# Kernel tuning notes

Measured on AMD Instinct MI355X. Metric: run time of the kernel, lower is better.

The kernel has to match this reference:

```python
import jax, jax.numpy as jnp
import numpy as np

N_NODES = 50000
N_EDGES = 640000
D_IN = 128
D_H1 = 128
D_H2 = 128
N_CLASSES = 64


def setup_inputs() -> dict:
    key = jax.random.key(0)
    ks = jax.random.split(key, 8)
    x = jax.random.normal(ks[0], (N_NODES, D_IN), dtype=jnp.float32)
    edge_index = jax.random.randint(ks[1], (2, N_EDGES), 0, N_NODES, dtype=jnp.int64)
    s1 = 1.0 / np.sqrt(D_IN)
    s2 = 1.0 / np.sqrt(D_H1)
    s3 = 1.0 / np.sqrt(D_H2)
    W1 = jax.random.uniform(ks[2], (D_IN, D_H1), jnp.float32, -s1, s1)
    b1 = jnp.zeros((D_H1,), jnp.float32)
    W2 = jax.random.uniform(ks[3], (D_H1, D_H2), jnp.float32, -s2, s2)
    b2 = jnp.zeros((D_H2,), jnp.float32)
    Wl = jax.random.uniform(ks[4], (D_H2, N_CLASSES), jnp.float32, -s3, s3)
    bl = jax.random.uniform(ks[5], (N_CLASSES,), jnp.float32, -s3, s3)
    return {"x": x, "edge_index": edge_index, "W1": W1, "b1": b1,
            "W2": W2, "b2": b2, "Wl": Wl, "bl": bl}


def _gcn_norm(edge_index, num_nodes):
    # PyG GCNConv: add self-loops, symmetric normalization D^-1/2 (A+I) D^-1/2
    loop = jnp.arange(num_nodes, dtype=edge_index.dtype)
    src = jnp.concatenate([edge_index[0], loop])
    dst = jnp.concatenate([edge_index[1], loop])
    deg = jax.ops.segment_sum(jnp.ones_like(dst, dtype=jnp.float32), dst,
                              num_segments=num_nodes)
    dinv = jnp.where(deg > 0, jax.lax.rsqrt(deg), 0.0)
    norm = dinv[src] * dinv[dst]  # [E+N]
    return src, dst, norm


def _gcn_conv(h, src, dst, norm, W, b, num_nodes):
    h = h @ W                       # transform first (smaller gather when D_out small)
    msg = h[src] * norm[:, None]    # gather + per-edge scale  [E+N, D_out]
    agg = jax.ops.segment_sum(msg, dst, num_segments=num_nodes)  # scatter-add
    return agg + b


def reference(x, edge_index, W1, b1, W2, b2, Wl, bl):
    n = x.shape[0]
    src, dst, norm = _gcn_norm(edge_index, n)
    h = jax.nn.relu(_gcn_conv(x, src, dst, norm, W1, b1, n))
    # dropout is identity in eval mode
    h = jax.nn.relu(_gcn_conv(h, src, dst, norm, W2, b2, n))
    return h @ Wl + bl
```

## Files before the change

### kernel.cpp

```cpp
#include <hip/hip_runtime.h>


typedef __attribute__((ext_vector_type(8))) __bf16 bf16x8;
typedef __attribute__((ext_vector_type(8))) short short8;
typedef __attribute__((ext_vector_type(4))) float f32x4;

__device__ inline float bf_lo(unsigned u) { return __uint_as_float(u << 16); }
__device__ inline float bf_hi(unsigned u) { return __uint_as_float(u & 0xffff0000u); }
__device__ inline unsigned short f2bf(float v) {
  return __builtin_bit_cast(unsigned short, (__bf16)v);
}

__global__ void k_count(const int* __restrict__ dst, int E,
                        int* __restrict__ cnt, int* __restrict__ rank) {
  int i = blockIdx.x * blockDim.x + threadIdx.x;
  if (i < E) rank[i] = atomicAdd(&cnt[dst[i]], 1);
}

__global__ void k_scan1_prepW(const int* __restrict__ cnt, int n, int* __restrict__ partial,
                              int nb,
                              const float* __restrict__ W1, const float* __restrict__ W2,
                              const float* __restrict__ Wl,
                              unsigned short* __restrict__ b1h, unsigned short* __restrict__ b1l,
                              unsigned short* __restrict__ b2h, unsigned short* __restrict__ b2l,
                              unsigned short* __restrict__ blh, unsigned short* __restrict__ bll) {
  if ((int)blockIdx.x < nb) {
    __shared__ int s[256];
    int i = blockIdx.x * 256 + threadIdx.x;
    s[threadIdx.x] = (i < n) ? cnt[i] : 0;
    __syncthreads();
    for (int off = 128; off > 0; off >>= 1) {
      if (threadIdx.x < off) s[threadIdx.x] += s[threadIdx.x + off];
      __syncthreads();
    }
    if (threadIdx.x == 0) partial[blockIdx.x] = s[0];
  } else {
    int idx = ((int)blockIdx.x - nb) * 256 + threadIdx.x;
    const float* W;
    unsigned short *bh, *bl_;
    int N, local;
    if (idx < 16384)      { W = W1; bh = b1h; bl_ = b1l; N = 128; local = idx; }
    else if (idx < 32768) { W = W2; bh = b2h; bl_ = b2l; N = 128; local = idx - 16384; }
    else if (idx < 40960) { W = Wl; bh = blh; bl_ = bll; N = 64;  local = idx - 32768; }
    else return;
    int nn = local >> 7, k = local & 127;
    float v = W[(size_t)k * N + nn];
    __bf16 h = (__bf16)v;
    bh[local] = __builtin_bit_cast(unsigned short, h);
    bl_[local] = f2bf(v - (float)h);
  }
}

__global__ void k_scan3(const int* __restrict__ cnt, const int* __restrict__ partial,
                        int nb, int n, int* __restrict__ row_off,
                        float* __restrict__ dinv) {
  __shared__ int s[256];
  __shared__ int base_s;
  int t = threadIdx.x;
  s[t] = (t < nb && t < (int)blockIdx.x) ? partial[t] : 0;
  __syncthreads();
  for (int off = 128; off > 0; off >>= 1) {
    if (t < off) s[t] += s[t + off];
    __syncthreads();
  }
  if (t == 0) base_s = s[0];
  __syncthreads();
  int base = base_s;
  __syncthreads();

  int i = blockIdx.x * 256 + t;
  int v = (i < n) ? cnt[i] : 0;
  s[t] = v;
  __syncthreads();
  for (int off = 1; off < 256; off <<= 1) {
    int u = (t >= off) ? s[t - off] : 0;
    __syncthreads();
    s[t] += u;
    __syncthreads();
  }
  int incl = s[t];
  int excl = incl - v;
  if (i < n) {
    row_off[i] = base + excl;
    dinv[i] = rsqrtf((float)(v + 1));
    if (i == n - 1) row_off[n] = base + incl;
  }
}

__global__ void k_place(const int* __restrict__ src, const int* __restrict__ dst,
                        const int* __restrict__ rank, const int* __restrict__ row_off,
                        int E, int* __restrict__ edges) {
  int e = blockIdx.x * blockDim.x + threadIdx.x;
  if (e < E) {
    int d = dst[e];
    int pos = row_off[d] + rank[e];
    __builtin_nontemporal_store(src[e], &edges[pos]);
  }
}

template <int NT, bool A32, bool BIAS, bool OUT_BF16, bool SCALE>
__global__ __launch_bounds__(256) void gemm3(
    const void* __restrict__ Ahi_, const unsigned short* __restrict__ Alo,
    const unsigned short* __restrict__ Bhi, const unsigned short* __restrict__ Blo,
    const float* __restrict__ bias, const float* __restrict__ dinv,
    void* __restrict__ Cout, int M) {
  constexpr int K = 128;
  constexpr int NCOL = NT * 16;
  __shared__ alignas(16) unsigned short lbh[NCOL * K];
  __shared__ alignas(16) unsigned short lbl[NCOL * K];
  int t = threadIdx.x;
  int lane = t & 63, wave = t >> 6;
  int lm = lane & 15, lk = lane >> 4;
  int m_base = blockIdx.x * 128 + wave * 32;
  const short8 zero8 = {0, 0, 0, 0, 0, 0, 0, 0};

  if (SCALE && blockIdx.x == 0 && t < 64) {
    *(unsigned*)&((unsigned short*)Cout)[(size_t)M * NCOL + t * 2] = 0u;
  }

  bf16x8 ah[2][4], al[2][4];
  if (A32) {
    const float* Af = (const float*)Ahi_;
    float4 ra[2][4][2];
#pragma unroll
    for (int mt = 0; mt < 2; ++mt) {
      int row = m_base + mt * 16 + lm;
#pragma unroll
      for (int ks = 0; ks < 4; ++ks) {
        if (row < M) {
          ra[mt][ks][0] = *(const float4*)&Af[(size_t)row * K + ks * 32 + lk * 8];
          ra[mt][ks][1] = *(const float4*)&Af[(size_t)row * K + ks * 32 + lk * 8 + 4];
        } else {
          ra[mt][ks][0] = make_float4(0.f, 0.f, 0.f, 0.f);
          ra[mt][ks][1] = make_float4(0.f, 0.f, 0.f, 0.f);
        }
      }
    }
#pragma unroll
    for (int mt = 0; mt < 2; ++mt)
#pragma unroll
      for (int ks = 0; ks < 4; ++ks) {
        float av[8] = {ra[mt][ks][0].x, ra[mt][ks][0].y, ra[mt][ks][0].z, ra[mt][ks][0].w,
                       ra[mt][ks][1].x, ra[mt][ks][1].y, ra[mt][ks][1].z, ra[mt][ks][1].w};
#pragma unroll
        for (int j = 0; j < 8; ++j) {
          __bf16 h = (__bf16)av[j];
          ah[mt][ks][j] = h;
          al[mt][ks][j] = (__bf16)(av[j] - (float)h);
        }
      }
  } else {
    const unsigned short* Ahi = (const unsigned short*)Ahi_;
#pragma unroll
    for (int mt = 0; mt < 2; ++mt) {
      int row = m_base + mt * 16 + lm;
#pragma unroll
      for (int ks = 0; ks < 4; ++ks) {
        if (row < M) {
          ah[mt][ks] = *(const bf16x8*)&Ahi[(size_t)row * K + ks * 32 + lk * 8];
          al[mt][ks] = *(const bf16x8*)&Alo[(size_t)row * K + ks * 32 + lk * 8];
        } else {
          ah[mt][ks] = __builtin_bit_cast(bf16x8, zero8);
          al[mt][ks] = __builtin_bit_cast(bf16x8, zero8);
        }
      }
    }
  }

  for (int c = t; c < NCOL * 16; c += 256) {
    int r = c >> 4, q = c & 15;
    int sq = q ^ (r & 15);
    *(short8*)&lbh[r * K + sq * 8] = *(const short8*)&Bhi[r * K + q * 8];
    *(short8*)&lbl[r * K + sq * 8] = *(const short8*)&Blo[r * K + q * 8];
  }
  __syncthreads();

  f32x4 acc[2][NT] = {};
#pragma unroll
  for (int ks = 0; ks < 4; ++ks) {
    int chunk = ks * 4 + lk;
    bf16x8 bh[NT], bl[NT];
#pragma unroll
    for (int nt = 0; nt < NT; ++nt) {
      int r = nt * 16 + lm;
      int sq = chunk ^ lm;
      bh[nt] = *(const bf16x8*)&lbh[r * K + sq * 8];
      bl[nt] = *(const bf16x8*)&lbl[r * K + sq * 8];
    }
#pragma unroll
    for (int mt = 0; mt < 2; ++mt)
#pragma unroll
      for (int nt = 0; nt < NT; ++nt) {
        acc[mt][nt] = __builtin_amdgcn_mfma_f32_16x16x32_bf16(ah[mt][ks], bh[nt], acc[mt][nt], 0, 0, 0);
        acc[mt][nt] = __builtin_amdgcn_mfma_f32_16x16x32_bf16(ah[mt][ks], bl[nt], acc[mt][nt], 0, 0, 0);
        acc[mt][nt] = __builtin_amdgcn_mfma_f32_16x16x32_bf16(al[mt][ks], bh[nt], acc[mt][nt], 0, 0, 0);
      }
  }

#pragma unroll
  for (int mt = 0; mt < 2; ++mt) {
#pragma unroll
    for (int r = 0; r < 4; ++r) {
      int row = m_base + mt * 16 + lk * 4 + r;
      if (row < M) {
        float dr = SCALE ? dinv[row] : 1.f;
#pragma unroll
        for (int nt = 0; nt < NT; ++nt) {
          int col = nt * 16 + lm;
          float v = acc[mt][nt][r];
          if (SCALE) v *= dr;
          if (BIAS) v += bias[col];
          if (OUT_BF16)
            ((unsigned short*)Cout)[(size_t)row * NCOL + col] = f2bf(v);
          else
            __builtin_nontemporal_store(v, &((float*)Cout)[(size_t)row * NCOL + col]);
        }
      }
    }
  }
}

__global__ __launch_bounds__(256) void k_agg(const unsigned short* __restrict__ t,
                      const int* __restrict__ row_off,
                      const int* __restrict__ edges,
                      const float* __restrict__ dinv, const float* __restrict__ bias,
                      unsigned short* __restrict__ ghi, unsigned short* __restrict__ glo,
                      int n) {
  int wave = threadIdx.x >> 6;
  int lane = threadIdx.x & 63;
  int g = lane >> 4;
  int fl = lane & 15;
  int node = blockIdx.x * 4 + wave;
  if (node >= n) return;
  int2 ro = *(const int2*)&row_off[node];
  int e0 = ro.x, e1 = ro.y;
  int last = e1 - 1;

  float acc[8] = {};
  for (int base = e0; base < e1; base += 8) {
    int i0 = base + g, i1 = base + 4 + g;
    int s0 = edges[i0 < e1 ? i0 : last];
    int s1 = edges[i1 < e1 ? i1 : last];
    s0 = i0 < e1 ? s0 : n;
    s1 = i1 < e1 ? s1 : n;
    uint4 u0 = *(const uint4*)&t[(size_t)s0 * 128 + fl * 8];
    uint4 u1 = *(const uint4*)&t[(size_t)s1 * 128 + fl * 8];
    acc[0] += bf_lo(u0.x) + bf_lo(u1.x);
    acc[1] += bf_hi(u0.x) + bf_hi(u1.x);
    acc[2] += bf_lo(u0.y) + bf_lo(u1.y);
    acc[3] += bf_hi(u0.y) + bf_hi(u1.y);
    acc[4] += bf_lo(u0.z) + bf_lo(u1.z);
    acc[5] += bf_hi(u0.z) + bf_hi(u1.z);
    acc[6] += bf_lo(u0.w) + bf_lo(u1.w);
    acc[7] += bf_hi(u0.w) + bf_hi(u1.w);
  }
#pragma unroll
  for (int j = 0; j < 8; ++j) {
    acc[j] += __shfl_xor(acc[j], 16);
    acc[j] += __shfl_xor(acc[j], 32);
  }
  if (g == 0) {
    float di = dinv[node];
    uint4 sv = *(const uint4*)&t[(size_t)node * 128 + fl * 8];
    acc[0] += bf_lo(sv.x); acc[1] += bf_hi(sv.x);
    acc[2] += bf_lo(sv.y); acc[3] += bf_hi(sv.y);
    acc[4] += bf_lo(sv.z); acc[5] += bf_hi(sv.z);
    acc[6] += bf_lo(sv.w); acc[7] += bf_hi(sv.w);
    float4 bb0 = *(const float4*)&bias[fl * 8];
    float4 bb1 = *(const float4*)&bias[fl * 8 + 4];
    float bb[8] = {bb0.x, bb0.y, bb0.z, bb0.w, bb1.x, bb1.y, bb1.z, bb1.w};
    short8 ho, lo_;
#pragma unroll
    for (int j = 0; j < 8; ++j) {
      float s = fmaxf(acc[j] * di + bb[j], 0.f);
      __bf16 h = (__bf16)s;
      ho[j] = __builtin_bit_cast(short, h);
      lo_[j] = (short)f2bf(s - (float)h);
    }
    *(short8*)&ghi[(size_t)node * 128 + fl * 8] = ho;
    *(short8*)&glo[(size_t)node * 128 + fl * 8] = lo_;
  }
}

extern "C" void kernel_launch(void* const* d_in, const int* in_sizes, int n_in,
                              void* d_out, int out_size, void* d_ws, size_t ws_size,
                              hipStream_t stream) {
  const float* x  = (const float*)d_in[0];
  const int*   ei = (const int*)d_in[1];
  const float* W1 = (const float*)d_in[2];
  const float* b1 = (const float*)d_in[3];
  const float* W2 = (const float*)d_in[4];
  const float* b2 = (const float*)d_in[5];
  const float* Wl = (const float*)d_in[6];
  const float* bl = (const float*)d_in[7];
  float* out = (float*)d_out;

  const int D = 128;
  int N = in_sizes[0] / D;
  int E = in_sizes[1] / 2;
  const int* src = ei;
  const int* dst = ei + E;

  uintptr_t ws = (uintptr_t)d_ws;
  auto take = [&](size_t bytes) {
    uintptr_t p = ws;
    ws += (bytes + 15) & ~(size_t)15;
    return p;
  };
  unsigned short* t_bf = (unsigned short*)take(((size_t)N + 1) * D * 2);
  unsigned short* xh   = (unsigned short*)take((size_t)N * D * 2);
  unsigned short* xl   = (unsigned short*)take((size_t)N * D * 2);
  int*   edges   = (int*)take((size_t)E * 4);
  int*   rank    = (int*)take((size_t)E * 4);
  int*   cnt     = (int*)take((size_t)N * sizeof(int));
  int*   row_off = (int*)take(((size_t)N + 1) * sizeof(int));
  float* dinv    = (float*)take((size_t)N * sizeof(float));
  int*   partial = (int*)take(256 * sizeof(int));
  unsigned short* b1h = (unsigned short*)take(128 * 128 * 2);
  unsigned short* b1l = (unsigned short*)take(128 * 128 * 2);
  unsigned short* b2h = (unsigned short*)take(128 * 128 * 2);
  unsigned short* b2l = (unsigned short*)take(128 * 128 * 2);
  unsigned short* blh = (unsigned short*)take(128 * 64 * 2);
  unsigned short* bll = (unsigned short*)take(128 * 64 * 2);

  int nb_n = (N + 255) / 256;
  int nb_e = (E + 255) / 256;

  hipMemsetAsync(cnt, 0, (size_t)N * sizeof(int), stream);
  k_count<<<nb_e, 256, 0, stream>>>(dst, E, cnt, rank);
  k_scan1_prepW<<<nb_n + 160, 256, 0, stream>>>(cnt, N, partial, nb_n,
                                                W1, W2, Wl, b1h, b1l, b2h, b2l, blh, bll);
  k_scan3<<<nb_n, 256, 0, stream>>>(cnt, partial, nb_n, N, row_off, dinv);
  k_place<<<nb_e, 256, 0, stream>>>(src, dst, rank, row_off, E, edges);

  int gemm_blocks = (N + 127) / 128;
  int agg_blocks = (N + 3) / 4;

  gemm3<8, true, false, true, true><<<gemm_blocks, 256, 0, stream>>>(
      x, nullptr, b1h, b1l, nullptr, dinv, t_bf, N);
  k_agg<<<agg_blocks, 256, 0, stream>>>(t_bf, row_off, edges, dinv, b1, xh, xl, N);
  gemm3<8, false, false, true, true><<<gemm_blocks, 256, 0, stream>>>(
      xh, xl, b2h, b2l, nullptr, dinv, t_bf, N);
  k_agg<<<agg_blocks, 256, 0, stream>>>(t_bf, row_off, edges, dinv, b2, xh, xl, N);
  gemm3<4, false, true, false, false><<<gemm_blocks, 256, 0, stream>>>(
      xh, xl, blh, bll, bl, nullptr, out, N);
}
```

Baseline: 234.8 us.

## Overlap first GEMM with edge counting and rescale with edge placement

The first-layer GEMM no longer depends on dinv. It runs in the same launch as the atomic degree counting, using extra auxiliary blocks. The dinv row scaling moves into a separate rescale pass, which runs in the same launch as the CSR edge placement. The memset is replaced by a kernel that also splits W1, so there are fewer launches and the independent stages run concurrently. In exchange, t_bf takes an extra read/write round trip, the row scale is applied to an already-rounded bf16 value, and the fused GEMM blocks use 64KB of LDS alongside the aux blocks.

```diff
diff --git a/kernel.cpp b/kernel.cpp
--- a/kernel.cpp
+++ b/kernel.cpp
@@ -11,17 +11,224 @@
   return __builtin_bit_cast(unsigned short, (__bf16)v);
 }
 
-__global__ void k_count(const int* __restrict__ dst, int E,
-                        int* __restrict__ cnt, int* __restrict__ rank) {
-  int i = blockIdx.x * blockDim.x + threadIdx.x;
-  if (i < E) rank[i] = atomicAdd(&cnt[dst[i]], 1);
+__device__ inline void prep_split(const float* __restrict__ W, int NN, int local,
+                                  unsigned short* __restrict__ bh,
+                                  unsigned short* __restrict__ bl_) {
+  int nn = local >> 7, k = local & 127;
+  float v = W[(size_t)k * NN + nn];
+  __bf16 h = (__bf16)v;
+  bh[local] = __builtin_bit_cast(unsigned short, h);
+  bl_[local] = f2bf(v - (float)h);
+}
+
+__global__ void k_init(int* __restrict__ cnt, int N,
+                       const float* __restrict__ W1,
+                       unsigned short* __restrict__ b1h, unsigned short* __restrict__ b1l) {
+  int nbz = (N + 255) / 256;
+  if ((int)blockIdx.x < nbz) {
+    int i = blockIdx.x * 256 + threadIdx.x;
+    if (i < N) cnt[i] = 0;
+  } else {
+    int idx = ((int)blockIdx.x - nbz) * 256 + threadIdx.x;
+    if (idx < 16384) prep_split(W1, 128, idx, b1h, b1l);
+  }
+}
+
+template <int NT, bool A32, bool BIAS, bool OUT_BF16, bool SCALE>
+__device__ void gemm_body(int bid,
+    const void* __restrict__ Ahi_, const unsigned short* __restrict__ Alo,
+    const unsigned short* __restrict__ Bhi, const unsigned short* __restrict__ Blo,
+    const float* __restrict__ bias, const float* __restrict__ dinv,
+    void* __restrict__ Cout, int M,
+    unsigned short* __restrict__ lbh, unsigned short* __restrict__ lbl) {
+  constexpr int K = 128;
+  constexpr int NCOL = NT * 16;
+  int t = threadIdx.x;
+  int lane = t & 63, wave = t >> 6;
+  int lm = lane & 15, lk = lane >> 4;
+  int m_base = bid * 128 + wave * 32;
+  const short8 zero8 = {0, 0, 0, 0, 0, 0, 0, 0};
+
+  bf16x8 ah[2][4], al[2][4];
+  if (A32) {
+    const float* Af = (const float*)Ahi_;
+    float4 ra[2][4][2];
+#pragma unroll
+    for (int mt = 0; mt < 2; ++mt) {
+      int row = m_base + mt * 16 + lm;
+#pragma unroll
+      for (int ks = 0; ks < 4; ++ks) {
+        if (row < M) {
+          ra[mt][ks][0] = *(const float4*)&Af[(size_t)row * K + ks * 32 + lk * 8];
+          ra[mt][ks][1] = *(const float4*)&Af[(size_t)row * K + ks * 32 + lk * 8 + 4];
+        } else {
+          ra[mt][ks][0] = make_float4(0.f, 0.f, 0.f, 0.f);
+          ra[mt][ks][1] = make_float4(0.f, 0.f, 0.f, 0.f);
+        }
+      }
+    }
+#pragma unroll
+    for (int mt = 0; mt < 2; ++mt)
+#pragma unroll
+      for (int ks = 0; ks < 4; ++ks) {
+        float av[8] = {ra[mt][ks][0].x, ra[mt][ks][0].y, ra[mt][ks][0].z, ra[mt][ks][0].w,
+                       ra[mt][ks][1].x, ra[mt][ks][1].y, ra[mt][ks][1].z, ra[mt][ks][1].w};
+#pragma unroll
+        for (int j = 0; j < 8; ++j) {
+          __bf16 h = (__bf16)av[j];
+          ah[mt][ks][j] = h;
+          al[mt][ks][j] = (__bf16)(av[j] - (float)h);
+        }
+      }
+  } else {
+    const unsigned short* Ahi = (const unsigned short*)Ahi_;
+#pragma unroll
+    for (int mt = 0; mt < 2; ++mt) {
+      int row = m_base + mt * 16 + lm;
+#pragma unroll
+      for (int ks = 0; ks < 4; ++ks) {
+        if (row < M) {
+          ah[mt][ks] = *(const bf16x8*)&Ahi[(size_t)row * K + ks * 32 + lk * 8];
+          al[mt][ks] = *(const bf16x8*)&Alo[(size_t)row * K + ks * 32 + lk * 8];
+        } else {
+          ah[mt][ks] = __builtin_bit_cast(bf16x8, zero8);
+          al[mt][ks] = __builtin_bit_cast(bf16x8, zero8);
+        }
+      }
+    }
+  }
+
+  for (int c = t; c < NCOL * 16; c += 256) {
+    int r = c >> 4, q = c & 15;
+    int sq = q ^ (r & 15);
+    *(short8*)&lbh[r * K + sq * 8] = *(const short8*)&Bhi[r * K + q * 8];
+    *(short8*)&lbl[r * K + sq * 8] = *(const short8*)&Blo[r * K + q * 8];
+  }
+  __syncthreads();
+
+  f32x4 acc[2][NT] = {};
+#pragma unroll
+  for (int ks = 0; ks < 4; ++ks) {
+    int chunk = ks * 4 + lk;
+    bf16x8 bh[NT], bl[NT];
+#pragma unroll
+    for (int nt = 0; nt < NT; ++nt) {
+      int r = nt * 16 + lm;
+      int sq = chunk ^ lm;
+      bh[nt] = *(const bf16x8*)&lbh[r * K + sq * 8];
+      bl[nt] = *(const bf16x8*)&lbl[r * K + sq * 8];
+    }
+#pragma unroll
+    for (int mt = 0; mt < 2; ++mt)
+#pragma unroll
+      for (int nt = 0; nt < NT; ++nt) {
+        acc[mt][nt] = __builtin_amdgcn_mfma_f32_16x16x32_bf16(ah[mt][ks], bh[nt], acc[mt][nt], 0, 0, 0);
+        acc[mt][nt] = __builtin_amdgcn_mfma_f32_16x16x32_bf16(ah[mt][ks], bl[nt], acc[mt][nt], 0, 0, 0);
+        acc[mt][nt] = __builtin_amdgcn_mfma_f32_16x16x32_bf16(al[mt][ks], bh[nt], acc[mt][nt], 0, 0, 0);
+      }
+  }
+
+#pragma unroll
+  for (int mt = 0; mt < 2; ++mt) {
+#pragma unroll
+    for (int r = 0; r < 4; ++r) {
+      int row = m_base + mt * 16 + lk * 4 + r;
+      if (row < M) {
+        float dr = SCALE ? dinv[row] : 1.f;
+#pragma unroll
+        for (int nt = 0; nt < NT; ++nt) {
+          int col = nt * 16 + lm;
+          float v = acc[mt][nt][r];
+          if (SCALE) v *= dr;
+          if (BIAS) v += bias[col];
+          if (OUT_BF16)
+            ((unsigned short*)Cout)[(size_t)row * NCOL + col] = f2bf(v);
+          else
+            __builtin_nontemporal_store(v, &((float*)Cout)[(size_t)row * NCOL + col]);
+        }
+      }
+    }
+  }
+}
+
+#define AUX_BLOCKS 512
+
+__global__ __launch_bounds__(256) void k_fat1(
+    const float* __restrict__ x,
+    const unsigned short* __restrict__ b1h, const unsigned short* __restrict__ b1l,
+    unsigned short* __restrict__ t_bf, int M, int G,
+    const int* __restrict__ dst, int E, int* __restrict__ cnt, int* __restrict__ rank) {
+  __shared__ alignas(16) unsigned short lbh[128 * 128];
+  __shared__ alignas(16) unsigned short lbl[128 * 128];
+  int b = blockIdx.x;
+  if (b < G) {
+    gemm_body<8, true, false, true, false>(b, x, nullptr, b1h, b1l,
+                                           nullptr, nullptr, t_bf, M, lbh, lbl);
+  } else {
+    for (int i = (b - G) * 256 + threadIdx.x; i < E; i += AUX_BLOCKS * 256)
+      rank[i] = atomicAdd(&cnt[dst[i]], 1);
+  }
+}
+
+__global__ __launch_bounds__(256) void k_fat2(
+    unsigned short* __restrict__ t_bf, const float* __restrict__ dinv, int N, int RB,
+    const int* __restrict__ src, const int* __restrict__ dst,
+    const int* __restrict__ rank, const int* __restrict__ row_off, int E,
+    int* __restrict__ edges) {
+  int b = blockIdx.x;
+  if (b < RB) {
+    int row = b * 8 + (threadIdx.x >> 5);
+    int seg = threadIdx.x & 31;
+    if (row < N) {
+      float d = dinv[row];
+      uint2 u = *(uint2*)&t_bf[(size_t)row * 128 + seg * 4];
+      ushort4 o;
+      o.x = f2bf(d * bf_lo(u.x));
+      o.y = f2bf(d * bf_hi(u.x));
+      o.z = f2bf(d * bf_lo(u.y));
+      o.w = f2bf(d * bf_hi(u.y));
+      *(ushort4*)&t_bf[(size_t)row * 128 + seg * 4] = o;
+    } else if (row == N) {
+      *(uint2*)&t_bf[(size_t)N * 128 + seg * 4] = make_uint2(0u, 0u);
+    }
+  } else {
+    for (int e = (b - RB) * 256 + threadIdx.x; e < E; e += AUX_BLOCKS * 256) {
+      int d = dst[e];
+      int pos = row_off[d] + rank[e];
+      __builtin_nontemporal_store(src[e], &edges[pos]);
+    }
+  }
+}
+
+template <int NT, bool A32, bool BIAS, bool OUT_BF16, bool SCALE>
+__global__ __launch_bounds__(256) void gemm3(
+    const void* __restrict__ Ahi_, const unsigned short* __restrict__ Alo,
+    const unsigned short* __restrict__ Bhi, const unsigned short* __restrict__ Blo,
+    const float* __restrict__ bias, const float* __restrict__ dinv,
+    void* __restrict__ Cout, int M) {
+  __shared__ alignas(16) unsigned short lbh[NT * 16 * 128];
+  __shared__ alignas(16) unsigned short lbl[NT * 16 * 128];
+  gemm_body<NT, A32, BIAS, OUT_BF16, SCALE>(blockIdx.x, Ahi_, Alo, Bhi, Blo,
+                                            bias, dinv, Cout, M, lbh, lbl);
+}
+
+template <int NT>
+__global__ __launch_bounds__(256) void gemm3_scale_zrow(
+    const unsigned short* __restrict__ Ahi, const unsigned short* __restrict__ Alo,
+    const unsigned short* __restrict__ Bhi, const unsigned short* __restrict__ Blo,
+    const float* __restrict__ dinv, unsigned short* __restrict__ Cout, int M) {
+  __shared__ alignas(16) unsigned short lbh[NT * 16 * 128];
+  __shared__ alignas(16) unsigned short lbl[NT * 16 * 128];
+  if (blockIdx.x == 0 && threadIdx.x < 64) {
+    *(unsigned*)&Cout[(size_t)M * NT * 16 + threadIdx.x * 2] = 0u;
+  }
+  gemm_body<NT, false, false, true, true>(blockIdx.x, Ahi, Alo, Bhi, Blo,
+                                          nullptr, dinv, Cout, M, lbh, lbl);
 }
 
 __global__ void k_scan1_prepW(const int* __restrict__ cnt, int n, int* __restrict__ partial,
                               int nb,
-                              const float* __restrict__ W1, const float* __restrict__ W2,
-                              const float* __restrict__ Wl,
-                              unsigned short* __restrict__ b1h, unsigned short* __restrict__ b1l,
+                              const float* __restrict__ W2, const float* __restrict__ Wl,
                               unsigned short* __restrict__ b2h, unsigned short* __restrict__ b2l,
                               unsigned short* __restrict__ blh, unsigned short* __restrict__ bll) {
   if ((int)blockIdx.x < nb) {
@@ -36,18 +243,8 @@
     if (threadIdx.x == 0) partial[blockIdx.x] = s[0];
   } else {
     int idx = ((int)blockIdx.x - nb) * 256 + threadIdx.x;
-    const float* W;
-    unsigned short *bh, *bl_;
-    int N, local;
-    if (idx < 16384)      { W = W1; bh = b1h; bl_ = b1l; N = 128; local = idx; }
-    else if (idx < 32768) { W = W2; bh = b2h; bl_ = b2l; N = 128; local = idx - 16384; }
-    else if (idx < 40960) { W = Wl; bh = blh; bl_ = bll; N = 64;  local = idx - 32768; }
-    else return;
-    int nn = local >> 7, k = local & 127;
-    float v = W[(size_t)k * N + nn];
-    __bf16 h = (__bf16)v;
-    bh[local] = __builtin_bit_cast(unsigned short, h);
-    bl_[local] = f2bf(v - (float)h);
+    if (idx < 16384)      prep_split(W2, 128, idx, b2h, b2l);
+    else if (idx < 24576) prep_split(Wl, 64, idx - 16384, blh, bll);
   }
 }
 
@@ -84,139 +281,6 @@
     row_off[i] = base + excl;
     dinv[i] = rsqrtf((float)(v + 1));
     if (i == n - 1) row_off[n] = base + incl;
-  }
-}
-
-__global__ void k_place(const int* __restrict__ src, const int* __restrict__ dst,
-                        const int* __restrict__ rank, const int* __restrict__ row_off,
-                        int E, int* __restrict__ edges) {
-  int e = blockIdx.x * blockDim.x + threadIdx.x;
-  if (e < E) {
-    int d = dst[e];
-    int pos = row_off[d] + rank[e];
-    __builtin_nontemporal_store(src[e], &edges[pos]);
-  }
-}
-
-template <int NT, bool A32, bool BIAS, bool OUT_BF16, bool SCALE>
-__global__ __launch_bounds__(256) void gemm3(
-    const void* __restrict__ Ahi_, const unsigned short* __restrict__ Alo,
-    const unsigned short* __restrict__ Bhi, const unsigned short* __restrict__ Blo,
-    const float* __restrict__ bias, const float* __restrict__ dinv,
-    void* __restrict__ Cout, int M) {
-  constexpr int K = 128;
-  constexpr int NCOL = NT * 16;
-  __shared__ alignas(16) unsigned short lbh[NCOL * K];
-  __shared__ alignas(16) unsigned short lbl[NCOL * K];
-  int t = threadIdx.x;
-  int lane = t & 63, wave = t >> 6;
-  int lm = lane & 15, lk = lane >> 4;
-  int m_base = blockIdx.x * 128 + wave * 32;
-  const short8 zero8 = {0, 0, 0, 0, 0, 0, 0, 0};
-
-  if (SCALE && blockIdx.x == 0 && t < 64) {
-    *(unsigned*)&((unsigned short*)Cout)[(size_t)M * NCOL + t * 2] = 0u;
-  }
-
-  bf16x8 ah[2][4], al[2][4];
-  if (A32) {
-    const float* Af = (const float*)Ahi_;
-    float4 ra[2][4][2];
-#pragma unroll
-    for (int mt = 0; mt < 2; ++mt) {
-      int row = m_base + mt * 16 + lm;
-#pragma unroll
-      for (int ks = 0; ks < 4; ++ks) {
-        if (row < M) {
-          ra[mt][ks][0] = *(const float4*)&Af[(size_t)row * K + ks * 32 + lk * 8];
-          ra[mt][ks][1] = *(const float4*)&Af[(size_t)row * K + ks * 32 + lk * 8 + 4];
-        } else {
-          ra[mt][ks][0] = make_float4(0.f, 0.f, 0.f, 0.f);
-          ra[mt][ks][1] = make_float4(0.f, 0.f, 0.f, 0.f);
-        }
-      }
-    }
-#pragma unroll
-    for (int mt = 0; mt < 2; ++mt)
-#pragma unroll
-      for (int ks = 0; ks < 4; ++ks) {
-        float av[8] = {ra[mt][ks][0].x, ra[mt][ks][0].y, ra[mt][ks][0].z, ra[mt][ks][0].w,
-                       ra[mt][ks][1].x, ra[mt][ks][1].y, ra[mt][ks][1].z, ra[mt][ks][1].w};
-#pragma unroll
-        for (int j = 0; j < 8; ++j) {
-          __bf16 h = (__bf16)av[j];
-          ah[mt][ks][j] = h;
-          al[mt][ks][j] = (__bf16)(av[j] - (float)h);
-        }
-      }
-  } else {
-    const unsigned short* Ahi = (const unsigned short*)Ahi_;
-#pragma unroll
-    for (int mt = 0; mt < 2; ++mt) {
-      int row = m_base + mt * 16 + lm;
-#pragma unroll
-      for (int ks = 0; ks < 4; ++ks) {
-        if (row < M) {
-          ah[mt][ks] = *(const bf16x8*)&Ahi[(size_t)row * K + ks * 32 + lk * 8];
-          al[mt][ks] = *(const bf16x8*)&Alo[(size_t)row * K + ks * 32 + lk * 8];
-        } else {
-          ah[mt][ks] = __builtin_bit_cast(bf16x8, zero8);
-          al[mt][ks] = __builtin_bit_cast(bf16x8, zero8);
-        }
-      }
-    }
-  }
-
-  for (int c = t; c < NCOL * 16; c += 256) {
-    int r = c >> 4, q = c & 15;
-    int sq = q ^ (r & 15);
-    *(short8*)&lbh[r * K + sq * 8] = *(const short8*)&Bhi[r * K + q * 8];
-    *(short8*)&lbl[r * K + sq * 8] = *(const short8*)&Blo[r * K + q * 8];
-  }
-  __syncthreads();
-
-  f32x4 acc[2][NT] = {};
-#pragma unroll
-  for (int ks = 0; ks < 4; ++ks) {
-    int chunk = ks * 4 + lk;
-    bf16x8 bh[NT], bl[NT];
-#pragma unroll
-    for (int nt = 0; nt < NT; ++nt) {
-      int r = nt * 16 + lm;
-      int sq = chunk ^ lm;
-      bh[nt] = *(const bf16x8*)&lbh[r * K + sq * 8];
-      bl[nt] = *(const bf16x8*)&lbl[r * K + sq * 8];
-    }
-#pragma unroll
-    for (int mt = 0; mt < 2; ++mt)
-#pragma unroll
-      for (int nt = 0; nt < NT; ++nt) {
-        acc[mt][nt] = __builtin_amdgcn_mfma_f32_16x16x32_bf16(ah[mt][ks], bh[nt], acc[mt][nt], 0, 0, 0);
-        acc[mt][nt] = __builtin_amdgcn_mfma_f32_16x16x32_bf16(ah[mt][ks], bl[nt], acc[mt][nt], 0, 0, 0);
-        acc[mt][nt] = __builtin_amdgcn_mfma_f32_16x16x32_bf16(al[mt][ks], bh[nt], acc[mt][nt], 0, 0, 0);
-      }
-  }
-
-#pragma unroll
-  for (int mt = 0; mt < 2; ++mt) {
-#pragma unroll
-    for (int r = 0; r < 4; ++r) {
-      int row = m_base + mt * 16 + lk * 4 + r;
-      if (row < M) {
-        float dr = SCALE ? dinv[row] : 1.f;
-#pragma unroll
-        for (int nt = 0; nt < NT; ++nt) {
-          int col = nt * 16 + lm;
-          float v = acc[mt][nt][r];
-          if (SCALE) v *= dr;
-          if (BIAS) v += bias[col];
-          if (OUT_BF16)
-            ((unsigned short*)Cout)[(size_t)row * NCOL + col] = f2bf(v);
-          else
-            __builtin_nontemporal_store(v, &((float*)Cout)[(size_t)row * NCOL + col]);
-        }
-      }
-    }
   }
 }
 
@@ -324,23 +388,20 @@
   unsigned short* bll = (unsigned short*)take(128 * 64 * 2);
 
   int nb_n = (N + 255) / 256;
-  int nb_e = (E + 255) / 256;
-
-  hipMemsetAsync(cnt, 0, (size_t)N * sizeof(int), stream);
-  k_count<<<nb_e, 256, 0, stream>>>(dst, E, cnt, rank);
-  k_scan1_prepW<<<nb_n + 160, 256, 0, stream>>>(cnt, N, partial, nb_n,
-                                                W1, W2, Wl, b1h, b1l, b2h, b2l, blh, bll);
-  k_scan3<<<nb_n, 256, 0, stream>>>(cnt, partial, nb_n, N, row_off, dinv);
-  k_place<<<nb_e, 256, 0, stream>>>(src, dst, rank, row_off, E, edges);
-
   int gemm_blocks = (N + 127) / 128;
   int agg_blocks = (N + 3) / 4;
-
-  gemm3<8, true, false, true, true><<<gemm_blocks, 256, 0, stream>>>(
-      x, nullptr, b1h, b1l, nullptr, dinv, t_bf, N);
+  int rescale_blocks = (N + 8) / 8;
+
+  k_init<<<nb_n + 64, 256, 0, stream>>>(cnt, N, W1, b1h, b1l);
+  k_fat1<<<gemm_blocks + AUX_BLOCKS, 256, 0, stream>>>(x, b1h, b1l, t_bf, N,
+                                                       gemm_blocks, dst, E, cnt, rank);
+  k_scan1_prepW<<<nb_n + 96, 256, 0, stream>>>(cnt, N, partial, nb_n,
+                                               W2, Wl, b2h, b2l, blh, bll);
+  k_scan3<<<nb_n, 256, 0, stream>>>(cnt, partial, nb_n, N, row_off, dinv);
+  k_fat2<<<rescale_blocks + AUX_BLOCKS, 256, 0, stream>>>(t_bf, dinv, N, rescale_blocks,
+                                                          src, dst, rank, row_off, E, edges);
   k_agg<<<agg_blocks, 256, 0, stream>>>(t_bf, row_off, edges, dinv, b1, xh, xl, N);
-  gemm3<8, false, false, true, true><<<gemm_blocks, 256, 0, stream>>>(
-      xh, xl, b2h, b2l, nullptr, dinv, t_bf, N);
+  gemm3_scale_zrow<8><<<gemm_blocks, 256, 0, stream>>>(xh, xl, b2h, b2l, dinv, t_bf, N);
   k_agg<<<agg_blocks, 256, 0, stream>>>(t_bf, row_off, edges, dinv, b2, xh, xl, N);
   gemm3<4, false, true, false, false><<<gemm_blocks, 256, 0, stream>>>(
       xh, xl, blh, bll, bl, nullptr, out, N);
```

Result: no change. 237.2 us (+1.0%).
